# Kernel optimization log

Hardware: AMD Instinct MI355X
Metric: run time of the kernel (lower is better)

The kernel has to match this reference:

```python
import jax, jax.numpy as jnp
import numpy as np

NEG = float(-2**32 + 1)
LN_EPS = 1e-5

def setup_inputs() -> dict:
    key = jax.random.key(0)
    ks = jax.random.split(key, 10)
    B, Sq, Sk, D = 8, 1024, 1024, 1024
    memory = jax.random.normal(ks[0], (B, Sk, D), jnp.float32)
    decoder_input = jax.random.normal(ks[1], (B, Sq, D), jnp.float32)
    query_mask = jax.random.uniform(ks[2], (B, Sq), jnp.float32)
    Wk = jax.random.normal(ks[3], (D, D), jnp.float32) * 0.02
    Wv = jax.random.normal(ks[4], (D, D), jnp.float32) * 0.02
    Wq = jax.random.normal(ks[5], (D, D), jnp.float32) * 0.02
    Wf = jax.random.normal(ks[6], (2 * D, D), jnp.float32) * 0.02
    bf = jnp.zeros((D,), jnp.float32)
    gamma = jnp.ones((D,), jnp.float32)
    beta = jnp.zeros((D,), jnp.float32)
    mask = jax.random.randint(ks[7], (B, Sq, Sk), 0, 2) == 1
    return dict(memory=memory, decoder_input=decoder_input, query_mask=query_mask,
                Wk=Wk, Wv=Wv, Wq=Wq, Wf=Wf, bf=bf, gamma=gamma, beta=beta, mask=mask)

def reference(memory, decoder_input, query_mask, Wk, Wv, Wq, Wf, bf, gamma, beta, mask):
    B, Sk, D = memory.shape
    Sq = decoder_input.shape[1]
    h = 8
    dh = D // h
    # projections (no bias), split heads -> [h, B, S, dh]
    K = (memory @ Wk).reshape(B, Sk, h, dh).transpose(2, 0, 1, 3)
    V = (memory @ Wv).reshape(B, Sk, h, dh).transpose(2, 0, 1, 3)
    Q = (decoder_input @ Wq).reshape(B, Sq, h, dh).transpose(2, 0, 1, 3)
    # scores [h, B, Sq, Sk]
    attn = jnp.einsum('hbqd,hbkd->hbqk', Q, K) / jnp.sqrt(jnp.float32(dh))
    attn = jnp.where(mask[None], NEG, attn)
    attn = jax.nn.softmax(attn, axis=-1)
    # non-standard post-softmax query-mask multiply
    attn = attn * query_mask[None, :, :, None]
    x = jnp.einsum('hbqk,hbkd->hbqd', attn, V)      # [h,B,Sq,dh]
    x = x.transpose(1, 2, 0, 3).reshape(B, Sq, D)    # concat heads
    x = jnp.concatenate([decoder_input, x], axis=-1)  # [B,Sq,2D]
    x = x @ Wf + bf
    x = x + decoder_input
    # LayerNorm
    mu = jnp.mean(x, axis=-1, keepdims=True)
    var = jnp.var(x, axis=-1, keepdims=True)
    x = (x - mu) * jax.lax.rsqrt(var + LN_EPS) * gamma + beta
    attns = attn.reshape(h * B, Sq, Sk)  # match torch layout [h*B,Sq,Sk]
    return x, attns
```

## Files before the change

kernel.cpp:

```cpp
#include <hip/hip_runtime.h>
#include <hip/hip_bf16.h>
#include <stdint.h>

typedef __attribute__((ext_vector_type(4))) float  floatx4;
typedef __attribute__((ext_vector_type(8))) short  shortx8;

__device__ __forceinline__ unsigned short f2bf(float f) {
    unsigned int u = __builtin_bit_cast(unsigned int, f);
    u += 0x7FFFu + ((u >> 16) & 1u);
    return (unsigned short)(u >> 16);
}
__device__ __forceinline__ float bf2f(unsigned short h) {
    unsigned int u = (unsigned int)h << 16;
    return __builtin_bit_cast(float, u);
}

__device__ __forceinline__ uint4 pack8(float4 a, float4 b) {
    uint4 r;
    r.x = (unsigned)f2bf(a.x) | ((unsigned)f2bf(a.y) << 16);
    r.y = (unsigned)f2bf(a.z) | ((unsigned)f2bf(a.w) << 16);
    r.z = (unsigned)f2bf(b.x) | ((unsigned)f2bf(b.y) << 16);
    r.w = (unsigned)f2bf(b.z) | ((unsigned)f2bf(b.w) << 16);
    return r;
}

__device__ __forceinline__ void gload16(const ushort* g, ushort* l) {
    __builtin_amdgcn_global_load_lds(
        (const __attribute__((address_space(1))) unsigned int*)g,
        (__attribute__((address_space(3))) unsigned int*)l, 16, 0, 0);
}

__global__ __launch_bounds__(256) void cast_pack(const float* __restrict__ mem,
                                                 const float* __restrict__ dec,
                                                 const int* __restrict__ mask,
                                                 ushort* __restrict__ mem_bf,
                                                 ushort* __restrict__ concat,
                                                 unsigned long long* __restrict__ mb) {
    int bx = blockIdx.x;
    if (bx < 4096) {
        long long i = ((long long)bx * 256 + threadIdx.x) * 8;
        const float4* p = (const float4*)(mem + i);
        *(uint4*)(mem_bf + i) = pack8(p[0], p[1]);
    } else if (bx < 8192) {
        long long i = ((long long)(bx - 4096) * 256 + threadIdx.x) * 8;
        long long r = i >> 10, c = i & 1023;
        const float4* p = (const float4*)(dec + i);
        *(uint4*)(concat + r * 2048 + c) = pack8(p[0], p[1]);
    } else {
        int gw = ((bx - 8192) * 256 + threadIdx.x) >> 6;
        int l = threadIdx.x & 63;
        #pragma unroll
        for (int i = 0; i < 16; ++i) {
            size_t widx = (size_t)gw * 16 + i;
            unsigned long long m = __ballot(mask[widx * 64 + l] != 0);
            if (l == 0) mb[widx] = m;
        }
    }
}

__global__ __launch_bounds__(256) void wtrans_all(const float* __restrict__ W0,
                                                  const float* __restrict__ W1,
                                                  const float* __restrict__ W2,
                                                  const float* __restrict__ W3,
                                                  ushort* __restrict__ T0,
                                                  ushort* __restrict__ T1,
                                                  ushort* __restrict__ T2,
                                                  ushort* __restrict__ T3) {
    __shared__ float t[32][33];
    int z = blockIdx.z;
    const float* W; ushort* WT; int K, byb;
    if (z == 0)      { W = W0; WT = T0; K = 1024; byb = blockIdx.y; }
    else if (z == 1) { W = W1; WT = T1; K = 1024; byb = blockIdx.y; }
    else if (z == 2) { W = W2; WT = T2; K = 1024; byb = blockIdx.y; }
    else             { W = W3; WT = T3; K = 2048; byb = blockIdx.y + (z - 3) * 32; }
    int tx = threadIdx.x, ty = threadIdx.y;
    int bx = blockIdx.x * 32;
    int by = byb * 32;
    #pragma unroll
    for (int i = 0; i < 4; i++)
        t[ty + 8 * i][tx] = W[(size_t)(by + ty + 8 * i) * 1024 + bx + tx];
    __syncthreads();
    #pragma unroll
    for (int i = 0; i < 4; i++)
        WT[(size_t)(bx + ty + 8 * i) * K + by + tx] = f2bf(t[tx][ty + 8 * i]);
}

__global__ __launch_bounds__(256) void vtrans(const ushort* __restrict__ V,
                                              ushort* __restrict__ VT) {
    __shared__ ushort t[32][33];
    int tx = threadIdx.x, ty = threadIdx.y;
    int bk = blockIdx.x * 32;
    int bd = blockIdx.y * 32;
    int z = blockIdx.z;
    int b = z >> 3, h = z & 7;
    #pragma unroll
    for (int i = 0; i < 4; i++)
        t[ty + 8 * i][tx] = V[((size_t)(b * 1024 + bk + ty + 8 * i)) * 1024 + h * 128 + bd + tx];
    __syncthreads();
    #pragma unroll
    for (int i = 0; i < 4; i++)
        VT[((size_t)((h * 8 + b) * 128 + bd + ty + 8 * i)) * 1024 + bk + tx] = t[tx][ty + 8 * i];
}

template <typename TC>
__device__ __forceinline__ void gemm_core(ushort* As, ushort* Bs,
                                          const ushort* __restrict__ A,
                                          const ushort* __restrict__ Bt, TC* __restrict__ C,
                                          int kbeg, int kend, int lda, int ldb, int ldc,
                                          int bm, int bn) {
    int tid = threadIdx.x;
    int l = tid & 63, wid = tid >> 6;
    int l16 = l & 15, quad = l >> 4;
    int wm = (wid & 1) * 64, wn = (wid >> 1) * 64;
    int srow = tid >> 3;
    int scol = (tid & 7) * 8;

    floatx4 acc[4][4];
    #pragma unroll
    for (int i = 0; i < 4; i++)
        #pragma unroll
        for (int j = 0; j < 4; j++)
            acc[i][j] = {0.0f, 0.0f, 0.0f, 0.0f};

    for (int kt = kbeg; kt < kend; kt += 64) {
        #pragma unroll
        for (int it = 0; it < 4; it++) {
            int row = it * 32 + srow;
            gload16(A + (size_t)(bm + row) * lda + kt + scol, &As[row * 64 + scol]);
            gload16(Bt + (size_t)(bn + row) * ldb + kt + scol, &Bs[row * 64 + scol]);
        }
        __syncthreads();
        #pragma unroll
        for (int kk = 0; kk < 64; kk += 32) {
            shortx8 af[4], bfr[4];
            #pragma unroll
            for (int i = 0; i < 4; i++)
                af[i] = *(const shortx8*)&As[(wm + i * 16 + l16) * 64 + kk + quad * 8];
            #pragma unroll
            for (int j = 0; j < 4; j++)
                bfr[j] = *(const shortx8*)&Bs[(wn + j * 16 + l16) * 64 + kk + quad * 8];
            #pragma unroll
            for (int i = 0; i < 4; i++)
                #pragma unroll
                for (int j = 0; j < 4; j++)
                    acc[i][j] = __builtin_amdgcn_mfma_f32_16x16x32_bf16(af[i], bfr[j], acc[i][j], 0, 0, 0);
        }
        __syncthreads();
    }

    #pragma unroll
    for (int i = 0; i < 4; i++) {
        #pragma unroll
        for (int j = 0; j < 4; j++) {
            int row0 = bm + wm + i * 16 + quad * 4;
            int col = bn + wn + j * 16 + l16;
            #pragma unroll
            for (int r = 0; r < 4; r++) {
                float v = acc[i][j][r];
                size_t idx = (size_t)(row0 + r) * ldc + col;
                if constexpr (__is_same(TC, float)) C[idx] = v;
                else C[idx] = f2bf(v);
            }
        }
    }
}

__global__ __launch_bounds__(256) void gemm_proj3(
    const ushort* __restrict__ mem_bf, const ushort* __restrict__ concat,
    const ushort* __restrict__ WkT, const ushort* __restrict__ WvT,
    const ushort* __restrict__ WqT,
    ushort* __restrict__ Kp, ushort* __restrict__ Vp, ushort* __restrict__ Qp) {
    __shared__ ushort As[128 * 64];
    __shared__ ushort Bs[128 * 64];
    int bid = blockIdx.x;
    int z = bid >> 9;
    int r = bid & 511;
    int xcd = r & 7, i = r >> 3;
    int m = xcd * 8 + (i & 7), n = i >> 3;
    const ushort* A; const ushort* Bt; ushort* C; int lda;
    if (z == 0)      { A = mem_bf; Bt = WkT; C = Kp; lda = 1024; }
    else if (z == 1) { A = mem_bf; Bt = WvT; C = Vp; lda = 1024; }
    else             { A = concat; Bt = WqT; C = Qp; lda = 2048; }
    gemm_core<ushort>(As, Bs, A, Bt, C, 0, 1024, lda, 1024, 1024, m * 128, n * 128);
}

__global__ __launch_bounds__(256) void gemm_ffn(
    const ushort* __restrict__ concat, const ushort* __restrict__ WfT,
    float* __restrict__ ffn0, float* __restrict__ ffn1) {
    __shared__ ushort As[128 * 64];
    __shared__ ushort Bs[128 * 64];
    int bid = blockIdx.x;
    int z = bid >> 9;
    int r = bid & 511;
    int xcd = r & 7, i = r >> 3;
    int m = xcd * 8 + (i & 7), n = i >> 3;
    gemm_core<float>(As, Bs, concat, WfT, z ? ffn1 : ffn0,
                     z * 1024, z * 1024 + 1024, 2048, 2048, 1024, m * 128, n * 128);
}

__global__ __launch_bounds__(256, 4) void fused_attn(
    const ushort* __restrict__ Qp, const ushort* __restrict__ Kp,
    const ushort* __restrict__ VT, const unsigned long long* __restrict__ mb,
    const float* __restrict__ qmask, float* __restrict__ attns,
    ushort* __restrict__ concat) {
    __shared__ ushort Qs[16 * 136];
    __shared__ ushort Ss[16 * 1032];
    __shared__ unsigned Ms[16][34];
    __shared__ float rowpart[16][5];
    __shared__ float scale_s[16];

    int bid = blockIdx.x;
    const int h = bid & 7;
    int t = bid >> 3;
    const int b = t >> 6;
    const int q0 = (t & 63) * 16;
    const int tid = threadIdx.x;
    const int w = tid >> 6, l = tid & 63;
    const int l16 = l & 15, quad = l >> 4;
    const float sc = 0.08838834764831845f;

    {
        int row = tid >> 4, col = (tid & 15) * 8;
        *(uint4*)&Qs[row * 136 + col] =
            *(const uint4*)(Qp + (size_t)(b * 1024 + q0 + row) * 1024 + h * 128 + col);
        int pr = tid & 15;
        uint2 mv = ((const uint2*)mb)[(size_t)(b * 1024 + q0 + row) * 16 + pr];
        Ms[row][pr * 2] = mv.x;
        Ms[row][pr * 2 + 1] = mv.y;
    }
    __syncthreads();

    shortx8 af[4];
    #pragma unroll
    for (int kk = 0; kk < 4; kk++)
        af[kk] = *(const shortx8*)&Qs[l16 * 136 + kk * 32 + quad * 8];

    const ushort* Kb = Kp + (size_t)(b * 1024 + w * 16 + l16) * 1024 + h * 128 + quad * 8;
#define KLD(c, o) (*(const shortx8*)(Kb + (size_t)(c) * 65536 + (o)))
    shortx8 ka0 = KLD(0, 0), ka1 = KLD(0, 32), ka2 = KLD(0, 64), ka3 = KLD(0, 96);
    shortx8 kb0 = KLD(1, 0), kb1 = KLD(1, 32), kb2 = KLD(1, 64), kb3 = KLD(1, 96);
    float ssum[4] = {0.0f, 0.0f, 0.0f, 0.0f};
    const int bp64 = w * 16 + l16;
    const int wsel = bp64 >> 5, bitp = bp64 & 31;
    #pragma unroll 1
    for (int cc = 0; cc < 16; cc += 2) {
        int c2 = cc + 2 < 16 ? cc + 2 : 14;
        int c3 = cc + 3 < 16 ? cc + 3 : 15;
        shortx8 n0 = KLD(c2, 0), n1 = KLD(c2, 32), n2 = KLD(c2, 64), n3 = KLD(c2, 96);
        floatx4 acc = {0.0f, 0.0f, 0.0f, 0.0f};
        __builtin_amdgcn_s_setprio(1);
        acc = __builtin_amdgcn_mfma_f32_16x16x32_bf16(af[0], ka0, acc, 0, 0, 0);
        acc = __builtin_amdgcn_mfma_f32_16x16x32_bf16(af[1], ka1, acc, 0, 0, 0);
        acc = __builtin_amdgcn_mfma_f32_16x16x32_bf16(af[2], ka2, acc, 0, 0, 0);
        acc = __builtin_amdgcn_mfma_f32_16x16x32_bf16(af[3], ka3, acc, 0, 0, 0);
        __builtin_amdgcn_s_setprio(0);
        {
            int k0 = cc * 64 + w * 16;
            #pragma unroll
            for (int r = 0; r < 4; ++r) {
                int q = quad * 4 + r;
                unsigned wv = Ms[q][cc * 2 + wsel];
                float v = ((wv >> bitp) & 1u) ? 0.0f : __expf(acc[r] * sc);
                ssum[r] += v;
                Ss[q * 1032 + k0 + l16] = f2bf(v);
            }
        }
        shortx8 m0 = KLD(c3, 0), m1 = KLD(c3, 32), m2 = KLD(c3, 64), m3 = KLD(c3, 96);
        floatx4 acc2 = {0.0f, 0.0f, 0.0f, 0.0f};
        __builtin_amdgcn_s_setprio(1);
        acc2 = __builtin_amdgcn_mfma_f32_16x16x32_bf16(af[0], kb0, acc2, 0, 0, 0);
        acc2 = __builtin_amdgcn_mfma_f32_16x16x32_bf16(af[1], kb1, acc2, 0, 0, 0);
        acc2 = __builtin_amdgcn_mfma_f32_16x16x32_bf16(af[2], kb2, acc2, 0, 0, 0);
        acc2 = __builtin_amdgcn_mfma_f32_16x16x32_bf16(af[3], kb3, acc2, 0, 0, 0);
        __builtin_amdgcn_s_setprio(0);
        {
            int k0 = (cc + 1) * 64 + w * 16;
            #pragma unroll
            for (int r = 0; r < 4; ++r) {
                int q = quad * 4 + r;
                unsigned wv = Ms[q][(cc + 1) * 2 + wsel];
                float v = ((wv >> bitp) & 1u) ? 0.0f : __expf(acc2[r] * sc);
                ssum[r] += v;
                Ss[q * 1032 + k0 + l16] = f2bf(v);
            }
        }
        ka0 = n0; ka1 = n1; ka2 = n2; ka3 = n3;
        kb0 = m0; kb1 = m1; kb2 = m2; kb3 = m3;
    }
#undef KLD

    #pragma unroll
    for (int r = 0; r < 4; ++r) {
        float s = ssum[r];
        #pragma unroll
        for (int off = 1; off < 16; off <<= 1) s += __shfl_xor(s, off, 16);
        ssum[r] = s;
    }
    if (l16 == 0) {
        #pragma unroll
        for (int r = 0; r < 4; ++r) rowpart[quad * 4 + r][w] = ssum[r];
    }
    __syncthreads();
    if (tid < 16) {
        float s = rowpart[tid][0] + rowpart[tid][1] + rowpart[tid][2] + rowpart[tid][3];
        scale_s[tid] = qmask[b * 1024 + q0 + tid] / s;
    }
    __syncthreads();

    const size_t vrow0 = (size_t)((h * 8 + b) * 128 + w * 32);
    const ushort* Vb0 = VT + (vrow0 + l16) * 1024 + quad * 8;
    const ushort* Vb1 = VT + (vrow0 + 16 + l16) * 1024 + quad * 8;
#define VLD(p, c, o) (*(const shortx8*)((p) + (c) * 64 + (o)))
    shortx8 va0 = VLD(Vb0, 0, 0), va1 = VLD(Vb1, 0, 0);
    shortx8 va2 = VLD(Vb0, 0, 32), va3 = VLD(Vb1, 0, 32);
    shortx8 vb0 = VLD(Vb0, 1, 0), vb1 = VLD(Vb1, 1, 0);
    shortx8 vb2 = VLD(Vb0, 1, 32), vb3 = VLD(Vb1, 1, 32);

    {
        int row = tid >> 4;
        float scl = scale_s[row];
        float* arow = attns + ((size_t)((h * 8 + b) * 1024 + q0 + row)) * 1024;
        int c0 = (tid & 15) * 4;
        #pragma unroll
        for (int j = 0; j < 16; ++j) {
            int c = c0 + j * 64;
            ushort4 v = *(const ushort4*)&Ss[row * 1032 + c];
            floatx4 o;
            o.x = bf2f(v.x) * scl;
            o.y = bf2f(v.y) * scl;
            o.z = bf2f(v.z) * scl;
            o.w = bf2f(v.w) * scl;
            __builtin_nontemporal_store(o, (floatx4*)(arow + c));
        }
    }

    floatx4 o0 = {0.0f, 0.0f, 0.0f, 0.0f}, o1 = {0.0f, 0.0f, 0.0f, 0.0f};
    #pragma unroll 1
    for (int cc = 0; cc < 16; cc += 2) {
        int c2 = cc + 2 < 16 ? cc + 2 : 14;
        int c3 = cc + 3 < 16 ? cc + 3 : 15;
        shortx8 n0 = VLD(Vb0, c2, 0), n1 = VLD(Vb1, c2, 0);
        shortx8 n2 = VLD(Vb0, c2, 32), n3 = VLD(Vb1, c2, 32);
        shortx8 pa0 = *(const shortx8*)&Ss[l16 * 1032 + cc * 64 + quad * 8];
        shortx8 pa1 = *(const shortx8*)&Ss[l16 * 1032 + cc * 64 + 32 + quad * 8];
        __builtin_amdgcn_s_setprio(1);
        o0 = __builtin_amdgcn_mfma_f32_16x16x32_bf16(pa0, va0, o0, 0, 0, 0);
        o1 = __builtin_amdgcn_mfma_f32_16x16x32_bf16(pa0, va1, o1, 0, 0, 0);
        o0 = __builtin_amdgcn_mfma_f32_16x16x32_bf16(pa1, va2, o0, 0, 0, 0);
        o1 = __builtin_amdgcn_mfma_f32_16x16x32_bf16(pa1, va3, o1, 0, 0, 0);
        __builtin_amdgcn_s_setprio(0);
        shortx8 m0 = VLD(Vb0, c3, 0), m1 = VLD(Vb1, c3, 0);
        shortx8 m2 = VLD(Vb0, c3, 32), m3 = VLD(Vb1, c3, 32);
        shortx8 pb0 = *(const shortx8*)&Ss[l16 * 1032 + (cc + 1) * 64 + quad * 8];
        shortx8 pb1 = *(const shortx8*)&Ss[l16 * 1032 + (cc + 1) * 64 + 32 + quad * 8];
        __builtin_amdgcn_s_setprio(1);
        o0 = __builtin_amdgcn_mfma_f32_16x16x32_bf16(pb0, vb0, o0, 0, 0, 0);
        o1 = __builtin_amdgcn_mfma_f32_16x16x32_bf16(pb0, vb1, o1, 0, 0, 0);
        o0 = __builtin_amdgcn_mfma_f32_16x16x32_bf16(pb1, vb2, o0, 0, 0, 0);
        o1 = __builtin_amdgcn_mfma_f32_16x16x32_bf16(pb1, vb3, o1, 0, 0, 0);
        __builtin_amdgcn_s_setprio(0);
        va0 = n0; va1 = n1; va2 = n2; va3 = n3;
        vb0 = m0; vb1 = m1; vb2 = m2; vb3 = m3;
    }
#undef VLD
    #pragma unroll
    for (int r = 0; r < 4; ++r) {
        int q = quad * 4 + r;
        float scl = scale_s[q];
        int d = w * 32 + l16;
        size_t base = (size_t)(b * 1024 + q0 + q) * 2048 + 1024 + h * 128;
        concat[base + d]      = f2bf(o0[r] * scl);
        concat[base + d + 16] = f2bf(o1[r] * scl);
    }
}

__global__ __launch_bounds__(256) void ln_out(const float* __restrict__ ffn0,
                                              const float* __restrict__ ffn1,
                                              const float* __restrict__ dec,
                                              const float* __restrict__ bfv,
                                              const float* __restrict__ gamma,
                                              const float* __restrict__ beta,
                                              float* __restrict__ out) {
    __shared__ float sb[8];
    int row = blockIdx.x, tid = threadIdx.x;
    int c = tid * 4;
    size_t base = (size_t)row * 1024 + c;
    float4 x = *(const float4*)(ffn0 + base);
    float4 y = *(const float4*)(ffn1 + base);
    float4 d = *(const float4*)(dec + base);
    float4 bb = *(const float4*)(bfv + c);
    x.x += y.x + d.x + bb.x; x.y += y.y + d.y + bb.y;
    x.z += y.z + d.z + bb.z; x.w += y.w + d.w + bb.w;

    float s = x.x + x.y + x.z + x.w;
    float s2 = x.x * x.x + x.y * x.y + x.z * x.z + x.w * x.w;
    #pragma unroll
    for (int o = 32; o; o >>= 1) {
        s += __shfl_down(s, o, 64);
        s2 += __shfl_down(s2, o, 64);
    }
    if ((tid & 63) == 0) { sb[tid >> 6] = s; sb[4 + (tid >> 6)] = s2; }
    __syncthreads();
    s = sb[0] + sb[1] + sb[2] + sb[3];
    s2 = sb[4] + sb[5] + sb[6] + sb[7];
    float mu = s * (1.0f / 1024.0f);
    float var = s2 * (1.0f / 1024.0f) - mu * mu;
    float rs = rsqrtf(var + 1e-5f);

    float4 g = *(const float4*)(gamma + c);
    float4 be = *(const float4*)(beta + c);
    float4 o4;
    o4.x = (x.x - mu) * rs * g.x + be.x;
    o4.y = (x.y - mu) * rs * g.y + be.y;
    o4.z = (x.z - mu) * rs * g.z + be.z;
    o4.w = (x.w - mu) * rs * g.w + be.w;
    *(float4*)(out + base) = o4;
}

extern "C" void kernel_launch(void* const* d_in, const int* in_sizes, int n_in,
                              void* d_out, int out_size, void* d_ws, size_t ws_size,
                              hipStream_t stream) {
    const float* memory  = (const float*)d_in[0];
    const float* decoder = (const float*)d_in[1];
    const float* qmask   = (const float*)d_in[2];
    const float* Wk      = (const float*)d_in[3];
    const float* Wv      = (const float*)d_in[4];
    const float* Wq      = (const float*)d_in[5];
    const float* Wf      = (const float*)d_in[6];
    const float* bfv     = (const float*)d_in[7];
    const float* gamma   = (const float*)d_in[8];
    const float* beta    = (const float*)d_in[9];
    const int*   mask    = (const int*)d_in[10];

    float* xout  = (float*)d_out;
    float* attns = xout + 8388608LL;

    char* w = (char*)d_ws;
    ushort* mem_bf = (ushort*)(w + 0);
    ushort* Kp     = (ushort*)(w + (16LL << 20));
    ushort* Qp     = (ushort*)(w + (32LL << 20));
    ushort* Vp     = (ushort*)(w + (48LL << 20));
    ushort* VT     = (ushort*)(w + (64LL << 20));
    ushort* concat = (ushort*)(w + (80LL << 20));
    ushort* WkT    = (ushort*)(w + (112LL << 20));
    ushort* WvT    = (ushort*)(w + (114LL << 20));
    ushort* WqT    = (ushort*)(w + (116LL << 20));
    ushort* WfT    = (ushort*)(w + (118LL << 20));
    unsigned long long* mbits = (unsigned long long*)(w + (122LL << 20));
    float* ffn0 = (float*)(w + 0);
    float* ffn1 = (float*)(w + (32LL << 20));

    cast_pack<<<10240, 256, 0, stream>>>(memory, decoder, mask, mem_bf, concat, mbits);
    wtrans_all<<<dim3(32, 32, 5), dim3(32, 8), 0, stream>>>(Wk, Wv, Wq, Wf, WkT, WvT, WqT, WfT);
    gemm_proj3<<<1536, 256, 0, stream>>>(mem_bf, concat, WkT, WvT, WqT, Kp, Vp, Qp);
    vtrans<<<dim3(32, 4, 64), dim3(32, 8), 0, stream>>>(Vp, VT);
    fused_attn<<<4096, 256, 0, stream>>>(Qp, Kp, VT, mbits, qmask, attns, concat);
    gemm_ffn<<<1024, 256, 0, stream>>>(concat, WfT, ffn0, ffn1);
    ln_out<<<8192, 256, 0, stream>>>(ffn0, ffn1, decoder, bfv, gamma, beta, xout);
}
```

Baseline: 770.7 us.

## Stage K and V tiles through double-buffered LDS in fused attention

```diff
diff --git a/kernel.cpp b/kernel.cpp
--- a/kernel.cpp
+++ b/kernel.cpp
@@ -198,13 +198,14 @@
                      z * 1024, z * 1024 + 1024, 2048, 2048, 1024, m * 128, n * 128);
 }
 
-__global__ __launch_bounds__(256, 4) void fused_attn(
+__global__ __launch_bounds__(256, 2) void fused_attn(
     const ushort* __restrict__ Qp, const ushort* __restrict__ Kp,
     const ushort* __restrict__ VT, const unsigned long long* __restrict__ mb,
     const float* __restrict__ qmask, float* __restrict__ attns,
     ushort* __restrict__ concat) {
     __shared__ ushort Qs[16 * 136];
     __shared__ ushort Ss[16 * 1032];
+    __shared__ ushort KV[2][8192];
     __shared__ unsigned Ms[16][34];
     __shared__ float rowpart[16][5];
     __shared__ float scale_s[16];
@@ -235,59 +236,64 @@
     for (int kk = 0; kk < 4; kk++)
         af[kk] = *(const shortx8*)&Qs[l16 * 136 + kk * 32 + quad * 8];
 
-    const ushort* Kb = Kp + (size_t)(b * 1024 + w * 16 + l16) * 1024 + h * 128 + quad * 8;
-#define KLD(c, o) (*(const shortx8*)(Kb + (size_t)(c) * 65536 + (o)))
-    shortx8 ka0 = KLD(0, 0), ka1 = KLD(0, 32), ka2 = KLD(0, 64), ka3 = KLD(0, 96);
-    shortx8 kb0 = KLD(1, 0), kb1 = KLD(1, 32), kb2 = KLD(1, 64), kb3 = KLD(1, 96);
+    const int ksrow = tid >> 4;
+    const int kscol = (tid & 15) * 8;
+    const ushort* Kbh = Kp + (size_t)b * 1048576 + h * 128;
+
+#define STAGE_K(c, buf)                                                          \
+    {                                                                            \
+        _Pragma("unroll")                                                        \
+        for (int rr = 0; rr < 4; ++rr)                                           \
+            gload16(Kbh + (size_t)((c) * 64 + rr * 16 + ksrow) * 1024 + kscol,   \
+                    &KV[buf][rr * 2048 + tid * 8]);                              \
+    }
+
     float ssum[4] = {0.0f, 0.0f, 0.0f, 0.0f};
     const int bp64 = w * 16 + l16;
     const int wsel = bp64 >> 5, bitp = bp64 & 31;
+    STAGE_K(0, 0);
+    __syncthreads();
+    int cur = 0;
     #pragma unroll 1
-    for (int cc = 0; cc < 16; cc += 2) {
-        int c2 = cc + 2 < 16 ? cc + 2 : 14;
-        int c3 = cc + 3 < 16 ? cc + 3 : 15;
-        shortx8 n0 = KLD(c2, 0), n1 = KLD(c2, 32), n2 = KLD(c2, 64), n3 = KLD(c2, 96);
+    for (int c = 0; c < 16; ++c) {
+        if (c < 15) STAGE_K(c + 1, cur ^ 1);
+        shortx8 b0 = *(const shortx8*)&KV[cur][(w * 16 + l16) * 128 + 0 * 32 + quad * 8];
+        shortx8 b1 = *(const shortx8*)&KV[cur][(w * 16 + l16) * 128 + 1 * 32 + quad * 8];
+        shortx8 b2 = *(const shortx8*)&KV[cur][(w * 16 + l16) * 128 + 2 * 32 + quad * 8];
+        shortx8 b3 = *(const shortx8*)&KV[cur][(w * 16 + l16) * 128 + 3 * 32 + quad * 8];
         floatx4 acc = {0.0f, 0.0f, 0.0f, 0.0f};
         __builtin_amdgcn_s_setprio(1);
-        acc = __builtin_amdgcn_mfma_f32_16x16x32_bf16(af[0], ka0, acc, 0, 0, 0);
-        acc = __builtin_amdgcn_mfma_f32_16x16x32_bf16(af[1], ka1, acc, 0, 0, 0);
-        acc = __builtin_amdgcn_mfma_f32_16x16x32_bf16(af[2], ka2, acc, 0, 0, 0);
-        acc = __builtin_amdgcn_mfma_f32_16x16x32_bf16(af[3], ka3, acc, 0, 0, 0);
+        acc = __builtin_amdgcn_mfma_f32_16x16x32_bf16(af[0], b0, acc, 0, 0, 0);
+        acc = __builtin_amdgcn_mfma_f32_16x16x32_bf16(af[1], b1, acc, 0, 0, 0);
+        acc = __builtin_amdgcn_mfma_f32_16x16x32_bf16(af[2], b2, acc, 0, 0, 0);
+        acc = __builtin_amdgcn_mfma_f32_16x16x32_bf16(af[3], b3, acc, 0, 0, 0);
         __builtin_amdgcn_s_setprio(0);
-        {
-            int k0 = cc * 64 + w * 16;
-            #pragma unroll
-            for (int r = 0; r < 4; ++r) {
-                int q = quad * 4 + r;
-                unsigned wv = Ms[q][cc * 2 + wsel];
-                float v = ((wv >> bitp) & 1u) ? 0.0f : __expf(acc[r] * sc);
-                ssum[r] += v;
-                Ss[q * 1032 + k0 + l16] = f2bf(v);
-            }
-        }
-        shortx8 m0 = KLD(c3, 0), m1 = KLD(c3, 32), m2 = KLD(c3, 64), m3 = KLD(c3, 96);
-        floatx4 acc2 = {0.0f, 0.0f, 0.0f, 0.0f};
-        __builtin_amdgcn_s_setprio(1);
-        acc2 = __builtin_amdgcn_mfma_f32_16x16x32_bf16(af[0], kb0, acc2, 0, 0, 0);
-        acc2 = __builtin_amdgcn_mfma_f32_16x16x32_bf16(af[1], kb1, acc2, 0, 0, 0);
-        acc2 = __builtin_amdgcn_mfma_f32_16x16x32_bf16(af[2], kb2, acc2, 0, 0, 0);
-        acc2 = __builtin_amdgcn_mfma_f32_16x16x32_bf16(af[3], kb3, acc2, 0, 0, 0);
-        __builtin_amdgcn_s_setprio(0);
-        {
-            int k0 = (cc + 1) * 64 + w * 16;
-            #pragma unroll
-            for (int r = 0; r < 4; ++r) {
-                int q = quad * 4 + r;
-                unsigned wv = Ms[q][(cc + 1) * 2 + wsel];
-                float v = ((wv >> bitp) & 1u) ? 0.0f : __expf(acc2[r] * sc);
-                ssum[r] += v;
-                Ss[q * 1032 + k0 + l16] = f2bf(v);
-            }
-        }
-        ka0 = n0; ka1 = n1; ka2 = n2; ka3 = n3;
-        kb0 = m0; kb1 = m1; kb2 = m2; kb3 = m3;
-    }
-#undef KLD
+        int k0 = c * 64 + w * 16;
+        #pragma unroll
+        for (int r = 0; r < 4; ++r) {
+            int q = quad * 4 + r;
+            unsigned wv = Ms[q][c * 2 + wsel];
+            float v = ((wv >> bitp) & 1u) ? 0.0f : __expf(acc[r] * sc);
+            ssum[r] += v;
+            Ss[q * 1032 + k0 + l16] = f2bf(v);
+        }
+        __syncthreads();
+        cur ^= 1;
+    }
+
+    const int vsrow = tid >> 3;
+    const int vscol = (tid & 7) * 8;
+    const ushort* Vbh = VT + (size_t)(h * 8 + b) * 131072;
+
+#define STAGE_V(c, buf)                                                          \
+    {                                                                            \
+        _Pragma("unroll")                                                        \
+        for (int rr = 0; rr < 4; ++rr)                                           \
+            gload16(Vbh + (size_t)(rr * 32 + vsrow) * 1024 + (c) * 64 + vscol,   \
+                    &KV[buf][rr * 2048 + tid * 8]);                              \
+    }
+
+    STAGE_V(0, 0);
 
     #pragma unroll
     for (int r = 0; r < 4; ++r) {
@@ -307,15 +313,36 @@
     }
     __syncthreads();
 
-    const size_t vrow0 = (size_t)((h * 8 + b) * 128 + w * 32);
-    const ushort* Vb0 = VT + (vrow0 + l16) * 1024 + quad * 8;
-    const ushort* Vb1 = VT + (vrow0 + 16 + l16) * 1024 + quad * 8;
-#define VLD(p, c, o) (*(const shortx8*)((p) + (c) * 64 + (o)))
-    shortx8 va0 = VLD(Vb0, 0, 0), va1 = VLD(Vb1, 0, 0);
-    shortx8 va2 = VLD(Vb0, 0, 32), va3 = VLD(Vb1, 0, 32);
-    shortx8 vb0 = VLD(Vb0, 1, 0), vb1 = VLD(Vb1, 1, 0);
-    shortx8 vb2 = VLD(Vb0, 1, 32), vb3 = VLD(Vb1, 1, 32);
-
+    floatx4 o0 = {0.0f, 0.0f, 0.0f, 0.0f}, o1 = {0.0f, 0.0f, 0.0f, 0.0f};
+    cur = 0;
+    #pragma unroll 1
+    for (int cc = 0; cc < 16; ++cc) {
+        if (cc < 15) STAGE_V(cc + 1, cur ^ 1);
+        shortx8 pa0 = *(const shortx8*)&Ss[l16 * 1032 + cc * 64 + quad * 8];
+        shortx8 pa1 = *(const shortx8*)&Ss[l16 * 1032 + cc * 64 + 32 + quad * 8];
+        shortx8 v00 = *(const shortx8*)&KV[cur][(w * 32 + l16) * 64 + 0 * 32 + quad * 8];
+        shortx8 v01 = *(const shortx8*)&KV[cur][(w * 32 + 16 + l16) * 64 + 0 * 32 + quad * 8];
+        shortx8 v10 = *(const shortx8*)&KV[cur][(w * 32 + l16) * 64 + 1 * 32 + quad * 8];
+        shortx8 v11 = *(const shortx8*)&KV[cur][(w * 32 + 16 + l16) * 64 + 1 * 32 + quad * 8];
+        __builtin_amdgcn_s_setprio(1);
+        o0 = __builtin_amdgcn_mfma_f32_16x16x32_bf16(pa0, v00, o0, 0, 0, 0);
+        o1 = __builtin_amdgcn_mfma_f32_16x16x32_bf16(pa0, v01, o1, 0, 0, 0);
+        o0 = __builtin_amdgcn_mfma_f32_16x16x32_bf16(pa1, v10, o0, 0, 0, 0);
+        o1 = __builtin_amdgcn_mfma_f32_16x16x32_bf16(pa1, v11, o1, 0, 0, 0);
+        __builtin_amdgcn_s_setprio(0);
+        __syncthreads();
+        cur ^= 1;
+    }
+
+    #pragma unroll
+    for (int r = 0; r < 4; ++r) {
+        int q = quad * 4 + r;
+        float scl = scale_s[q];
+        int d = w * 32 + l16;
+        size_t base = (size_t)(b * 1024 + q0 + q) * 2048 + 1024 + h * 128;
+        concat[base + d]      = f2bf(o0[r] * scl);
+        concat[base + d + 16] = f2bf(o1[r] * scl);
+    }
     {
         int row = tid >> 4;
         float scl = scale_s[row];
@@ -332,45 +359,6 @@
             o.w = bf2f(v.w) * scl;
             __builtin_nontemporal_store(o, (floatx4*)(arow + c));
         }
-    }
-
-    floatx4 o0 = {0.0f, 0.0f, 0.0f, 0.0f}, o1 = {0.0f, 0.0f, 0.0f, 0.0f};
-    #pragma unroll 1
-    for (int cc = 0; cc < 16; cc += 2) {
-        int c2 = cc + 2 < 16 ? cc + 2 : 14;
-        int c3 = cc + 3 < 16 ? cc + 3 : 15;
-        shortx8 n0 = VLD(Vb0, c2, 0), n1 = VLD(Vb1, c2, 0);
-        shortx8 n2 = VLD(Vb0, c2, 32), n3 = VLD(Vb1, c2, 32);
-        shortx8 pa0 = *(const shortx8*)&Ss[l16 * 1032 + cc * 64 + quad * 8];
-        shortx8 pa1 = *(const shortx8*)&Ss[l16 * 1032 + cc * 64 + 32 + quad * 8];
-        __builtin_amdgcn_s_setprio(1);
-        o0 = __builtin_amdgcn_mfma_f32_16x16x32_bf16(pa0, va0, o0, 0, 0, 0);
-        o1 = __builtin_amdgcn_mfma_f32_16x16x32_bf16(pa0, va1, o1, 0, 0, 0);
-        o0 = __builtin_amdgcn_mfma_f32_16x16x32_bf16(pa1, va2, o0, 0, 0, 0);
-        o1 = __builtin_amdgcn_mfma_f32_16x16x32_bf16(pa1, va3, o1, 0, 0, 0);
-        __builtin_amdgcn_s_setprio(0);
-        shortx8 m0 = VLD(Vb0, c3, 0), m1 = VLD(Vb1, c3, 0);
-        shortx8 m2 = VLD(Vb0, c3, 32), m3 = VLD(Vb1, c3, 32);
-        shortx8 pb0 = *(const shortx8*)&Ss[l16 * 1032 + (cc + 1) * 64 + quad * 8];
-        shortx8 pb1 = *(const shortx8*)&Ss[l16 * 1032 + (cc + 1) * 64 + 32 + quad * 8];
-        __builtin_amdgcn_s_setprio(1);
-        o0 = __builtin_amdgcn_mfma_f32_16x16x32_bf16(pb0, vb0, o0, 0, 0, 0);
-        o1 = __builtin_amdgcn_mfma_f32_16x16x32_bf16(pb0, vb1, o1, 0, 0, 0);
-        o0 = __builtin_amdgcn_mfma_f32_16x16x32_bf16(pb1, vb2, o0, 0, 0, 0);
-        o1 = __builtin_amdgcn_mfma_f32_16x16x32_bf16(pb1, vb3, o1, 0, 0, 0);
-        __builtin_amdgcn_s_setprio(0);
-        va0 = n0; va1 = n1; va2 = n2; va3 = n3;
-        vb0 = m0; vb1 = m1; vb2 = m2; vb3 = m3;
-    }
-#undef VLD
-    #pragma unroll
-    for (int r = 0; r < 4; ++r) {
-        int q = quad * 4 + r;
-        float scl = scale_s[q];
-        int d = w * 32 + l16;
-        size_t base = (size_t)(b * 1024 + q0 + q) * 2048 + 1024 + h * 128;
-        concat[base + d]      = f2bf(o0[r] * scl);
-        concat[base + d + 16] = f2bf(o1[r] * scl);
     }
 }
 
```

Measured after the change: 752.0 us. 2.4% less time.
